# Optimization experiments

Measured on AMD Instinct MI355X. Metric: run time of the kernel, lower is better.

Reference implementation:

```python
import jax, jax.numpy as jnp
import numpy as np

N = 200000          # total nodes
G = 512             # num graphs (segments)
D = 256             # in_dim == h_dim == sum_dim
OUT = 128           # head out_dim
L = 4               # depth
EPS = 1e-5


def setup_inputs() -> dict:
    key = jax.random.key(0)
    ks = jax.random.split(key, 12)
    x = jax.random.normal(ks[0], (N, D), dtype=jnp.float32)
    batch = jnp.sort(jax.random.randint(ks[1], (N,), 0, G)).astype(jnp.int32)
    s = 0.06  # ~xavier scale for 256-wide layers
    return {
        "x": x,
        "batch": batch,
        "phi_w1": s * jax.random.normal(ks[2], (L, D, D), dtype=jnp.float32),
        "phi_b1": jnp.zeros((L, D), jnp.float32),
        "phi_ln_g": jnp.ones((L, D), jnp.float32),
        "phi_ln_b": jnp.zeros((L, D), jnp.float32),
        "phi_w2": s * jax.random.normal(ks[3], (L, D, D), dtype=jnp.float32),
        "phi_b2": jnp.zeros((L, D), jnp.float32),
        "psi_w1": s * jax.random.normal(ks[4], (L, 2 * D, D), dtype=jnp.float32),
        "psi_b1": jnp.zeros((L, D), jnp.float32),
        "psi_ln_g": jnp.ones((L, D), jnp.float32),
        "psi_ln_b": jnp.zeros((L, D), jnp.float32),
        "psi_w2": s * jax.random.normal(ks[5], (L, D, D), dtype=jnp.float32),
        "psi_b2": jnp.zeros((L, D), jnp.float32),
        "out_ln_g": jnp.ones((L, D), jnp.float32),
        "out_ln_b": jnp.zeros((L, D), jnp.float32),
        "head_w": s * jax.random.normal(ks[6], (D, OUT), dtype=jnp.float32),
        "head_b": jnp.zeros((OUT,), jnp.float32),
    }


def _ln(h, g, b):
    mu = jnp.mean(h, axis=-1, keepdims=True)
    var = jnp.mean(jnp.square(h - mu), axis=-1, keepdims=True)
    return (h - mu) * jax.lax.rsqrt(var + EPS) * g + b


def _mlp(h, w1, b1, g, beta, w2, b2):
    # Linear -> ReLU -> LayerNorm -> Linear (MLP with num_layers=2, use_ln=True)
    h = jax.nn.relu(h @ w1 + b1)
    h = _ln(h, g, beta)
    return h @ w2 + b2


def reference(x, batch, phi_w1, phi_b1, phi_ln_g, phi_ln_b, phi_w2, phi_b2,
              psi_w1, psi_b1, psi_ln_g, psi_ln_b, psi_w2, psi_b2,
              out_ln_g, out_ln_b, head_w, head_b):
    for i in range(L):
        phi_x = _mlp(x, phi_w1[i], phi_b1[i], phi_ln_g[i], phi_ln_b[i], phi_w2[i], phi_b2[i])
        # global_add_pool: scatter-add per graph, then gather back to nodes
        gsum = jax.ops.segment_sum(phi_x, batch, num_segments=G)   # [G, D]
        expanded = gsum[batch]                                      # [N, D]
        combined = jnp.concatenate([x, expanded], axis=-1)          # [N, 2D]
        out = _mlp(combined, psi_w1[i], psi_b1[i], psi_ln_g[i], psi_ln_b[i], psi_w2[i], psi_b2[i])
        out = x + out                                               # residual (in_dim == out_dim)
        x = _ln(out, out_ln_g[i], out_ln_b[i])                      # out_ln
    return x @ head_w + head_b
```

## Files before the change

### kernel.cpp

```cpp
#include <hip/hip_runtime.h>
#include <stdint.h>

#define DEV __device__ __forceinline__

constexpr int NN = 200000;
constexpr int GSEG = 512;

typedef __attribute__((ext_vector_type(8)))  short   s8v;
typedef __attribute__((ext_vector_type(4)))  float   f4v;
typedef __attribute__((ext_vector_type(16))) float   f16v;
typedef __attribute__((ext_vector_type(4)))  unsigned short u4v;
typedef __attribute__((ext_vector_type(4)))  _Float16 h4v;

DEV void mfma32(const s8v& a, const s8v& b, f16v& c){
  asm volatile("v_mfma_f32_32x32x16_bf16 %0, %1, %2, %0" : "+v"(c) : "v"(a), "v"(b));
}

DEV unsigned short f2bs(float f){
  union { float f; uint32_t u; } v; v.f = f;
  uint32_t u = v.u;
  u = u + 0x7fffu + ((u >> 16) & 1u);
  return (unsigned short)(u >> 16);
}
DEV float b2f(unsigned short s){
  union { uint32_t u; float f; } v; v.u = ((uint32_t)s) << 16;
  return v.f;
}
DEV unsigned short f2h(float f){
  union{ _Float16 h; unsigned short u; } v; v.h = (_Float16)f; return v.u;
}
DEV s8v cvt8(f4v a, f4v b){
  s8v r;
  r[0]=(short)f2bs(a[0]); r[1]=(short)f2bs(a[1]); r[2]=(short)f2bs(a[2]); r[3]=(short)f2bs(a[3]);
  r[4]=(short)f2bs(b[0]); r[5]=(short)f2bs(b[1]); r[6]=(short)f2bs(b[2]); r[7]=(short)f2bs(b[3]);
  return r;
}

DEV void gload_lds16(const void* g, void* l){
  __builtin_amdgcn_global_load_lds(
      (const __attribute__((address_space(1))) void*)g,
      (__attribute__((address_space(3))) void*)l, 16, 0, 0);
}

template<int BSRC>
DEV s8v load_bfrag(const unsigned short* Xb, const float* Xf, const float* gsum,
                   int row, int g, int kk, int k16){
  if constexpr(BSRC==0){
    return *(const s8v*)(Xb + (size_t)row*256 + kk);
  } else if constexpr(BSRC==1){
    const float* p = Xf + (size_t)row*256 + kk;
    return cvt8(*(const f4v*)p, *(const f4v*)(p+4));
  } else {
    if(k16 < 16){
      if constexpr(BSRC==2){
        return *(const s8v*)(Xb + (size_t)row*256 + kk);
      } else {
        const float* p = Xf + (size_t)row*256 + kk;
        return cvt8(*(const f4v*)p, *(const f4v*)(p+4));
      }
    } else {
      const float* p = gsum + (size_t)g*256 + (kk - 256);
      return cvt8(*(const f4v*)p, *(const f4v*)(p+4));
    }
  }
}

template<int DOUT,int KDIM,int BSRC,int MODE,int RES,int WRH>
__global__ __launch_bounds__(256,2) void gemm_ln(
    const unsigned short* Xb, const float* Xf, const float* gsumIn, const int* batch,
    const unsigned short* PW, const float* bias, const float* lng, const float* lnb,
    const float* xresf, const unsigned short* xresh, const unsigned short* xresb,
    unsigned short* outb, unsigned short* outh, float* outf)
{
  constexpr int NM  = DOUT/32;
  constexpr int NI  = DOUT/64;
  constexpr int CHB = NM*4096;
  constexpr int ITER= CHB/4096;
  __shared__ __align__(16) char smem[CHB + 2048];
  __shared__ __align__(16) char sT[32768];

  const int tid  = threadIdx.x;
  const int lane = tid & 63;
  const int wid  = tid >> 6;
  const int wr = wid >> 1, wc = wid & 1;
  const int l32 = lane & 31, h = lane >> 5;
  const int rb   = (int)blockIdx.x * 128;
  const int row0 = rb + wr*64 + l32;
  const int row1 = row0 + 32;
  const int r0c = row0 < NN ? row0 : NN-1;
  const int r1c = row1 < NN ? row1 : NN-1;

  f16v acc[2][NI];
  #pragma unroll
  for(int ni=0; ni<NI; ++ni){
    #pragma unroll
    for(int rq=0; rq<4; ++rq){
      f4v bv = *(const f4v*)(bias + wc*(DOUT/2) + ni*32 + 8*rq + 4*h);
      #pragma unroll
      for(int j=0;j<4;++j){ acc[0][ni][rq*4+j]=bv[j]; acc[1][ni][rq*4+j]=bv[j]; }
    }
  }

  int g0=0, g1=0;
  if constexpr(BSRC>=2){ g0 = batch[r0c]; g1 = batch[r1c]; }

  for(int kc=0; kc<KDIM/64; ++kc){
    const unsigned short* src = PW + (size_t)kc*(CHB/2);
    #pragma unroll
    for(int it=0; it<ITER; ++it){
      int idx = it*256 + tid;
      gload_lds16(src + (size_t)idx*8, smem + (it*256 + wid*64)*16);
    }
    __syncthreads();
    #pragma unroll
    for(int k2=0;k2<4;++k2){
      const int k16 = kc*4 + k2;
      const int kk  = k16*16 + h*8;
      s8v b0 = load_bfrag<BSRC>(Xb, Xf, gsumIn, r0c, g0, kk, k16);
      s8v b1 = load_bfrag<BSRC>(Xb, Xf, gsumIn, r1c, g1, kk, k16);
      #pragma unroll
      for(int ni=0; ni<NI; ++ni){
        s8v a = *(const s8v*)(smem + ((k2*NM + wc*NI + ni)*64 + lane)*16);
        mfma32(a, b0, acc[0][ni]);
        mfma32(a, b1, acc[1][ni]);
      }
    }
    __syncthreads();
  }

  if constexpr(MODE==0 || MODE==1){
    #pragma unroll
    for(int nj=0;nj<2;++nj){
      if constexpr(MODE==1){
        const int rr = nj ? r1c : r0c;
        #pragma unroll
        for(int ni=0;ni<NI;++ni){
          #pragma unroll
          for(int rq=0;rq<4;++rq){
            const int c4 = wc*(DOUT/2) + ni*32 + 8*rq + 4*h;
            f4v rv;
            if constexpr(RES==1){
              rv = *(const f4v*)(xresf + (size_t)rr*256 + c4);
            } else if constexpr(RES==2){
              h4v hv = *(const h4v*)(xresh + (size_t)rr*256 + c4);
              #pragma unroll
              for(int j=0;j<4;++j) rv[j] = (float)hv[j];
            } else {
              u4v u = *(const u4v*)(xresb + (size_t)rr*256 + c4);
              #pragma unroll
              for(int j=0;j<4;++j) rv[j] = b2f(u[j]);
            }
            #pragma unroll
            for(int j=0;j<4;++j) acc[nj][ni][rq*4+j] += rv[j];
          }
        }
      } else {
        #pragma unroll
        for(int ni=0;ni<NI;++ni)
          #pragma unroll
          for(int r=0;r<16;++r) acc[nj][ni][r] = fmaxf(acc[nj][ni][r], 0.f);
      }
    }
    float s[2]={0.f,0.f}, q[2]={0.f,0.f};
    #pragma unroll
    for(int nj=0;nj<2;++nj)
      #pragma unroll
      for(int ni=0;ni<NI;++ni)
        #pragma unroll
        for(int r=0;r<16;++r){ float v = acc[nj][ni][r]; s[nj]+=v; q[nj]=fmaf(v,v,q[nj]); }
    #pragma unroll
    for(int nj=0;nj<2;++nj){ s[nj] += __shfl_xor(s[nj],32); q[nj] += __shfl_xor(q[nj],32); }
    float2* st = (float2*)(smem + CHB);
    if(lane < 32){
      st[(((wr*2+0)*32)+lane)*2 + wc] = make_float2(s[0], q[0]);
      st[(((wr*2+1)*32)+lane)*2 + wc] = make_float2(s[1], q[1]);
    }
    __syncthreads();
    float mu[2], rs[2];
    #pragma unroll
    for(int nj=0;nj<2;++nj){
      f4v v = *(const f4v*)(st + (((wr*2+nj)*32)+l32)*2);
      float S = v[0]+v[2], Q = v[1]+v[3];
      mu[nj] = S*(1.f/256.f);
      float var = Q*(1.f/256.f) - mu[nj]*mu[nj];
      rs[nj] = rsqrtf(var + 1e-5f);
    }
    for(int chunk=0; chunk<2; ++chunk){
      if(chunk) __syncthreads();
      if(wr == chunk){
        #pragma unroll
        for(int nj=0;nj<2;++nj){
          #pragma unroll
          for(int ni=0;ni<NI;++ni){
            #pragma unroll
            for(int rq=0;rq<4;++rq){
              const int c4 = wc*(DOUT/2) + ni*32 + 8*rq + 4*h;
              f4v gv = *(const f4v*)(lng + c4);
              f4v bv = *(const f4v*)(lnb + c4);
              u4v o;
              #pragma unroll
              for(int j=0;j<4;++j)
                o[j] = f2bs(fmaf((acc[nj][ni][rq*4+j]-mu[nj])*rs[nj], gv[j], bv[j]));
              *(u4v*)(sT + (nj*32+l32)*512 + ((c4*2) ^ (l32<<4))) = o;
            }
          }
        }
      }
      __syncthreads();
      #pragma unroll
      for(int i=0;i<8;++i){
        const int r = i*8 + (tid>>5);
        const int c = tid & 31;
        const int grow = rb + chunk*64 + r;
        if(grow < NN)
          *(s8v*)(outb + (size_t)grow*256 + c*8) =
              *(const s8v*)(sT + r*512 + ((c*16) ^ ((r&31)<<4)));
      }
    }
    if constexpr(WRH){
      for(int chunk=0; chunk<2; ++chunk){
        __syncthreads();
        if(wr == chunk){
          #pragma unroll
          for(int nj=0;nj<2;++nj){
            #pragma unroll
            for(int ni=0;ni<NI;++ni){
              #pragma unroll
              for(int rq=0;rq<4;++rq){
                const int c4 = wc*(DOUT/2) + ni*32 + 8*rq + 4*h;
                f4v gv = *(const f4v*)(lng + c4);
                f4v bv = *(const f4v*)(lnb + c4);
                u4v o;
                #pragma unroll
                for(int j=0;j<4;++j)
                  o[j] = f2h(fmaf((acc[nj][ni][rq*4+j]-mu[nj])*rs[nj], gv[j], bv[j]));
                *(u4v*)(sT + (nj*32+l32)*512 + ((c4*2) ^ (l32<<4))) = o;
              }
            }
          }
        }
        __syncthreads();
        #pragma unroll
        for(int i=0;i<8;++i){
          const int r = i*8 + (tid>>5);
          const int c = tid & 31;
          const int grow = rb + chunk*64 + r;
          if(grow < NN)
            *(s8v*)(outh + (size_t)grow*256 + c*8) =
                *(const s8v*)(sT + r*512 + ((c*16) ^ ((r&31)<<4)));
        }
      }
    }
  } else {
    for(int chunk=0; chunk<2; ++chunk){
      if(chunk) __syncthreads();
      if(wr == chunk){
        #pragma unroll
        for(int nj=0;nj<2;++nj){
          #pragma unroll
          for(int ni=0;ni<NI;++ni){
            #pragma unroll
            for(int rq=0;rq<4;++rq){
              const int c4 = wc*(DOUT/2) + ni*32 + 8*rq + 4*h;
              f4v o;
              #pragma unroll
              for(int j=0;j<4;++j) o[j] = acc[nj][ni][rq*4+j];
              *(f4v*)(sT + (nj*32+l32)*512 + ((c4*4) ^ (l32<<4))) = o;
            }
          }
        }
      }
      __syncthreads();
      #pragma unroll
      for(int i=0;i<8;++i){
        const int r = i*8 + (tid>>5);
        const int c = tid & 31;
        const int grow = rb + chunk*64 + r;
        if(grow < NN)
          *(f4v*)(outf + (size_t)grow*DOUT + c*4) =
              *(const f4v*)(sT + r*512 + ((c*16) ^ ((r&31)<<4)));
      }
    }
  }
}

__global__ __launch_bounds__(256,2) void gemm_segsum(
    const unsigned short* Xb, const unsigned short* PW, const float* bias,
    const int* batch, float* gsum)
{
  __shared__ __align__(16) char smem[32768];
  const int tid = threadIdx.x, lane = tid&63, wid = tid>>6;
  const int wr = wid>>1, wc = wid&1, l32 = lane&31, h = lane>>5;
  const int rb = (int)blockIdx.x*128;
  const int ra0 = rb + wr*64 + l32;
  const int ra1 = ra0 + 32;
  const int r0c = ra0 < NN ? ra0 : NN-1;
  const int r1c = ra1 < NN ? ra1 : NN-1;
  const int browi = rb + wr*64 + lane;
  const int b_l = (browi < NN) ? batch[browi] : 0x7fffffff;

  f16v acc[2][4];
  #pragma unroll
  for(int n=0;n<4;++n){
    float bv = bias[wc*128 + n*32 + l32];
    #pragma unroll
    for(int m=0;m<2;++m)
      #pragma unroll
      for(int r=0;r<16;++r) acc[m][n][r] = bv;
  }

  for(int kc=0; kc<4; ++kc){
    const unsigned short* src = PW + (size_t)kc*16384;
    #pragma unroll
    for(int it=0; it<8; ++it){
      int idx = it*256 + tid;
      gload_lds16(src + (size_t)idx*8, smem + (it*256 + wid*64)*16);
    }
    __syncthreads();
    #pragma unroll
    for(int k2=0;k2<4;++k2){
      const int kk = (kc*4+k2)*16 + h*8;
      s8v a0 = *(const s8v*)(Xb + (size_t)r0c*256 + kk);
      s8v a1 = *(const s8v*)(Xb + (size_t)r1c*256 + kk);
      #pragma unroll
      for(int n=0;n<4;++n){
        s8v bw = *(const s8v*)(smem + ((k2*8 + wc*4 + n)*64 + lane)*16);
        mfma32(a0, bw, acc[0][n]);
        mfma32(a1, bw, acc[1][n]);
      }
    }
    __syncthreads();
  }

  int lo = 0;
  while(lo < 64){
    int g = __shfl(b_l, lo);
    unsigned long long mb = __ballot(b_l == g);
    int hi = lo + __popcll(mb);
    if(g < GSEG){
      #pragma unroll
      for(int n=0;n<4;++n){
        float sum = 0.f;
        #pragma unroll
        for(int m=0;m<2;++m){
          if(hi <= m*32 || lo >= m*32+32) continue;
          #pragma unroll
          for(int r=0;r<16;++r){
            int lr = m*32 + (r&3) + 8*(r>>2) + 4*h;
            sum += (lr >= lo && lr < hi) ? acc[m][n][r] : 0.f;
          }
        }
        sum += __shfl_xor(sum, 32);
        if(lane < 32) atomicAdd(&gsum[(size_t)g*256 + wc*128 + n*32 + lane], sum);
      }
    }
    lo = hi;
  }
}

__global__ void pack_weights(const float* phi_w1, const float* phi_w2,
                             const float* psi_w1, const float* psi_w2,
                             const float* head_w, unsigned short* pw)
{
  int o = (int)blockIdx.x*256 + (int)threadIdx.x;
  if(o >= 167936) return;
  const float* src; unsigned short* dst; int Dout, oo;
  if(o < 32768){        int l=o>>13;            oo=o&8191;  src=phi_w1+(size_t)l*65536;  dst=pw+(size_t)l*65536;           Dout=256; }
  else if(o < 65536){   int t=o-32768,l=t>>13;  oo=t&8191;  src=phi_w2+(size_t)l*65536;  dst=pw+262144+(size_t)l*65536;    Dout=256; }
  else if(o < 131072){  int t=o-65536,l=t>>14;  oo=t&16383; src=psi_w1+(size_t)l*131072; dst=pw+524288+(size_t)l*131072;   Dout=256; }
  else if(o < 163840){  int t=o-131072,l=t>>13; oo=t&8191;  src=psi_w2+(size_t)l*65536;  dst=pw+1048576+(size_t)l*65536;   Dout=256; }
  else{                 oo=o-163840;            src=head_w; dst=pw+1310720;                                                Dout=128; }
  const int NM = Dout/32;
  int lane = oo & 63;
  int m   = (oo>>6) % NM;
  int k16 = (oo>>6) / NM;
  int kb  = k16*16 + (lane>>5)*8;
  int col = m*32 + (lane&31);
  #pragma unroll
  for(int jj=0;jj<8;++jj) dst[(size_t)oo*8 + jj] = f2bs(src[(size_t)(kb+jj)*Dout + col]);
}

extern "C" void kernel_launch(void* const* d_in, const int* in_sizes, int n_in,
                              void* d_out, int out_size, void* d_ws, size_t ws_size,
                              hipStream_t stream)
{
  (void)in_sizes; (void)n_in; (void)out_size;
  const float* x0       = (const float*)d_in[0];
  const int*   batch    = (const int*)  d_in[1];
  const float* phi_w1   = (const float*)d_in[2];
  const float* phi_b1   = (const float*)d_in[3];
  const float* phi_ln_g = (const float*)d_in[4];
  const float* phi_ln_b = (const float*)d_in[5];
  const float* phi_w2   = (const float*)d_in[6];
  const float* phi_b2   = (const float*)d_in[7];
  const float* psi_w1   = (const float*)d_in[8];
  const float* psi_b1   = (const float*)d_in[9];
  const float* psi_ln_g = (const float*)d_in[10];
  const float* psi_ln_b = (const float*)d_in[11];
  const float* psi_w2   = (const float*)d_in[12];
  const float* psi_b2   = (const float*)d_in[13];
  const float* out_ln_g = (const float*)d_in[14];
  const float* out_ln_b = (const float*)d_in[15];
  const float* head_w   = (const float*)d_in[16];
  const float* head_b   = (const float*)d_in[17];

  char* ws = (char*)d_ws;
  unsigned short* pw = (unsigned short*)ws;
  float* gsum        = (float*)(ws + 4194304);
  unsigned short* hb = (unsigned short*)(ws + 8388608);
  const bool dual = (ws_size >= 315588608ull);
  unsigned short* xb = dual ? (unsigned short*)(ws + 110788608)
                            : (unsigned short*)d_out;
  unsigned short* xh = dual ? (unsigned short*)(ws + 213188608) : nullptr;

  const int grid = (NN + 127)/128;

  pack_weights<<<656,256,0,stream>>>(phi_w1, phi_w2, psi_w1, psi_w2, head_w, pw);

  for(int l=0;l<4;++l){
    const unsigned short* pw_phi1 = pw + (size_t)l*65536;
    const unsigned short* pw_phi2 = pw + 262144 + (size_t)l*65536;
    const unsigned short* pw_psi1 = pw + 524288 + (size_t)l*131072;
    const unsigned short* pw_psi2 = pw + 1048576 + (size_t)l*65536;
    const float* b1 = phi_b1 + l*256, *g1 = phi_ln_g + l*256, *n1 = phi_ln_b + l*256;
    const float* b2 = phi_b2 + l*256;
    const float* p1 = psi_b1 + l*256, *pg = psi_ln_g + l*256, *pn = psi_ln_b + l*256;
    const float* p2 = psi_b2 + l*256;
    const float* og = out_ln_g + l*256, *on = out_ln_b + l*256;

    if(l==0)
      gemm_ln<256,256,1,0,0,0><<<grid,256,0,stream>>>(nullptr, x0, nullptr, nullptr,
          pw_phi1, b1, g1, n1, nullptr, nullptr, nullptr, hb, nullptr, nullptr);
    else
      gemm_ln<256,256,0,0,0,0><<<grid,256,0,stream>>>(xb, nullptr, nullptr, nullptr,
          pw_phi1, b1, g1, n1, nullptr, nullptr, nullptr, hb, nullptr, nullptr);

    hipMemsetAsync(gsum, 0, 524288, stream);
    gemm_segsum<<<grid,256,0,stream>>>(hb, pw_phi2, b2, batch, gsum);

    if(l==0)
      gemm_ln<256,512,3,0,0,0><<<grid,256,0,stream>>>(nullptr, x0, gsum, batch,
          pw_psi1, p1, pg, pn, nullptr, nullptr, nullptr, hb, nullptr, nullptr);
    else
      gemm_ln<256,512,2,0,0,0><<<grid,256,0,stream>>>(xb, nullptr, gsum, batch,
          pw_psi1, p1, pg, pn, nullptr, nullptr, nullptr, hb, nullptr, nullptr);

    if(l==0){
      if(dual)
        gemm_ln<256,256,0,1,1,1><<<grid,256,0,stream>>>(hb, nullptr, nullptr, nullptr,
            pw_psi2, p2, og, on, x0, nullptr, nullptr, xb, xh, nullptr);
      else
        gemm_ln<256,256,0,1,1,0><<<grid,256,0,stream>>>(hb, nullptr, nullptr, nullptr,
            pw_psi2, p2, og, on, x0, nullptr, nullptr, xb, nullptr, nullptr);
    } else if(l<3){
      if(dual)
        gemm_ln<256,256,0,1,2,1><<<grid,256,0,stream>>>(hb, nullptr, nullptr, nullptr,
            pw_psi2, p2, og, on, nullptr, xh, nullptr, xb, xh, nullptr);
      else
        gemm_ln<256,256,0,1,3,0><<<grid,256,0,stream>>>(hb, nullptr, nullptr, nullptr,
            pw_psi2, p2, og, on, nullptr, nullptr, xb, xb, nullptr, nullptr);
    } else {
      if(dual)
        gemm_ln<256,256,0,1,2,0><<<grid,256,0,stream>>>(hb, nullptr, nullptr, nullptr,
            pw_psi2, p2, og, on, nullptr, xh, nullptr, xb, nullptr, nullptr);
      else
        gemm_ln<256,256,0,1,3,0><<<grid,256,0,stream>>>(hb, nullptr, nullptr, nullptr,
            pw_psi2, p2, og, on, nullptr, nullptr, xb, xb, nullptr, nullptr);
    }
  }

  gemm_ln<128,256,0,2,0,0><<<grid,256,0,stream>>>(xb, nullptr, nullptr, nullptr,
      pw + 1310720, head_b, nullptr, nullptr, nullptr, nullptr, nullptr,
      nullptr, nullptr, (float*)d_out);
}
```

Measured before the change: 1.698 ms.

## Store bf16/fp16 activations in MFMA-fragment tiled layout, drop LDS transpose epilogue

Intermediate bf16/fp16 activations move from row-major to a tiled layout (32-row blocks, 8-element column groups contiguous per row). B-fragment loads then become fully coalesced 512-byte runs, and the LN epilogue can write results straight from registers, pairing halves with a cross-lane shuffle. This removes the LDS staging buffer and its barriers in non-MODE2 kernels and cuts LDS usage, which may allow higher occupancy. The cost is that every producer and consumer must agree on the new layout, and the residual reads and other kernels have to be updated to match.

After: 1.516 ms. 10.7% less time.

```diff
diff --git a/kernel.cpp b/kernel.cpp
--- a/kernel.cpp
+++ b/kernel.cpp
@@ -42,26 +42,34 @@
       (__attribute__((address_space(3))) void*)l, 16, 0, 0);
 }
 
+DEV u4v shfl_xor32_u4(u4v v){
+  union { u4v q; long long l; } a, b;
+  a.q = v;
+  b.l = __shfl_xor(a.l, 32);
+  return b.q;
+}
+
+
 template<int BSRC>
 DEV s8v load_bfrag(const unsigned short* Xb, const float* Xf, const float* gsum,
-                   int row, int g, int kk, int k16){
+                   int row, int g, int k16, int h){
   if constexpr(BSRC==0){
-    return *(const s8v*)(Xb + (size_t)row*256 + kk);
+    return *(const s8v*)(Xb + (size_t)(row>>5)*8192 + (size_t)(k16*2+h)*256 + (row&31)*8);
   } else if constexpr(BSRC==1){
-    const float* p = Xf + (size_t)row*256 + kk;
+    const float* p = Xf + (size_t)row*256 + k16*16 + h*8;
+    return cvt8(*(const f4v*)p, *(const f4v*)(p+4));
+  } else if constexpr(BSRC==2){
+    if(k16 < 16)
+      return *(const s8v*)(Xb + (size_t)(row>>5)*8192 + (size_t)(k16*2+h)*256 + (row&31)*8);
+    const float* p = gsum + (size_t)g*256 + (k16-16)*16 + h*8;
     return cvt8(*(const f4v*)p, *(const f4v*)(p+4));
   } else {
     if(k16 < 16){
-      if constexpr(BSRC==2){
-        return *(const s8v*)(Xb + (size_t)row*256 + kk);
-      } else {
-        const float* p = Xf + (size_t)row*256 + kk;
-        return cvt8(*(const f4v*)p, *(const f4v*)(p+4));
-      }
-    } else {
-      const float* p = gsum + (size_t)g*256 + (kk - 256);
+      const float* p = Xf + (size_t)row*256 + k16*16 + h*8;
       return cvt8(*(const f4v*)p, *(const f4v*)(p+4));
     }
+    const float* p = gsum + (size_t)g*256 + (k16-16)*16 + h*8;
+    return cvt8(*(const f4v*)p, *(const f4v*)(p+4));
   }
 }
 
@@ -77,7 +85,7 @@
   constexpr int CHB = NM*4096;
   constexpr int ITER= CHB/4096;
   __shared__ __align__(16) char smem[CHB + 2048];
-  __shared__ __align__(16) char sT[32768];
+  __shared__ __align__(16) char sT[(MODE==2) ? 32768 : 16];
 
   const int tid  = threadIdx.x;
   const int lane = tid & 63;
@@ -115,9 +123,8 @@
     #pragma unroll
     for(int k2=0;k2<4;++k2){
       const int k16 = kc*4 + k2;
-      const int kk  = k16*16 + h*8;
-      s8v b0 = load_bfrag<BSRC>(Xb, Xf, gsumIn, r0c, g0, kk, k16);
-      s8v b1 = load_bfrag<BSRC>(Xb, Xf, gsumIn, r1c, g1, kk, k16);
+      s8v b0 = load_bfrag<BSRC>(Xb, Xf, gsumIn, r0c, g0, k16, h);
+      s8v b1 = load_bfrag<BSRC>(Xb, Xf, gsumIn, r1c, g1, k16, h);
       #pragma unroll
       for(int ni=0; ni<NI; ++ni){
         s8v a = *(const s8v*)(smem + ((k2*NM + wc*NI + ni)*64 + lane)*16);
@@ -142,11 +149,13 @@
             if constexpr(RES==1){
               rv = *(const f4v*)(xresf + (size_t)rr*256 + c4);
             } else if constexpr(RES==2){
-              h4v hv = *(const h4v*)(xresh + (size_t)rr*256 + c4);
+              const int o = wc*16 + ni*4 + rq;
+              h4v hv = *(const h4v*)(xresh + (size_t)(rr>>5)*8192 + (size_t)o*256 + (rr&31)*8 + 4*h);
               #pragma unroll
               for(int j=0;j<4;++j) rv[j] = (float)hv[j];
             } else {
-              u4v u = *(const u4v*)(xresb + (size_t)rr*256 + c4);
+              const int o = wc*16 + ni*4 + rq;
+              u4v u = *(const u4v*)(xresb + (size_t)(rr>>5)*8192 + (size_t)o*256 + (rr&31)*8 + 4*h);
               #pragma unroll
               for(int j=0;j<4;++j) rv[j] = b2f(u[j]);
             }
@@ -185,69 +194,61 @@
       float var = Q*(1.f/256.f) - mu[nj]*mu[nj];
       rs[nj] = rsqrtf(var + 1e-5f);
     }
-    for(int chunk=0; chunk<2; ++chunk){
-      if(chunk) __syncthreads();
-      if(wr == chunk){
-        #pragma unroll
-        for(int nj=0;nj<2;++nj){
-          #pragma unroll
-          for(int ni=0;ni<NI;++ni){
+    #pragma unroll
+    for(int nj=0;nj<2;++nj){
+      const int rowS = nj ? row1 : row0;
+      #pragma unroll
+      for(int t=0;t<8;++t){
+        const int niE = (16*t)>>5,     rqE = (2*t)&3;
+        const int niO = (16*t+8)>>5,   rqO = (2*t+1)&3;
+        f4v fe, fo;
+        {
+          const int c4 = wc*(DOUT/2) + niE*32 + 8*rqE + 4*h;
+          f4v gv = *(const f4v*)(lng + c4);
+          f4v bv = *(const f4v*)(lnb + c4);
+          #pragma unroll
+          for(int j=0;j<4;++j)
+            fe[j] = fmaf((acc[nj][niE][rqE*4+j]-mu[nj])*rs[nj], gv[j], bv[j]);
+        }
+        {
+          const int c4 = wc*(DOUT/2) + niO*32 + 8*rqO + 4*h;
+          f4v gv = *(const f4v*)(lng + c4);
+          f4v bv = *(const f4v*)(lnb + c4);
+          #pragma unroll
+          for(int j=0;j<4;++j)
+            fo[j] = fmaf((acc[nj][niO][rqO*4+j]-mu[nj])*rs[nj], gv[j], bv[j]);
+        }
+        const int o = wc*16 + 2*t + h;
+        unsigned short* dst = outb + (size_t)(rowS>>5)*8192 + (size_t)o*256 + (rowS&31)*8;
+        {
+          u4v qe, qo;
+          #pragma unroll
+          for(int j=0;j<4;++j){ qe[j] = f2bs(fe[j]); qo[j] = f2bs(fo[j]); }
+          u4v snd = h ? qe : qo;
+          u4v rcv = shfl_xor32_u4(snd);
+          u4v lo4 = h ? rcv : qe;
+          u4v hi4 = h ? qo  : rcv;
+          if(rowS < NN){
+            s8v ov;
             #pragma unroll
-            for(int rq=0;rq<4;++rq){
-              const int c4 = wc*(DOUT/2) + ni*32 + 8*rq + 4*h;
-              f4v gv = *(const f4v*)(lng + c4);
-              f4v bv = *(const f4v*)(lnb + c4);
-              u4v o;
-              #pragma unroll
-              for(int j=0;j<4;++j)
-                o[j] = f2bs(fmaf((acc[nj][ni][rq*4+j]-mu[nj])*rs[nj], gv[j], bv[j]));
-              *(u4v*)(sT + (nj*32+l32)*512 + ((c4*2) ^ (l32<<4))) = o;
-            }
+            for(int j=0;j<4;++j){ ov[j] = (short)lo4[j]; ov[4+j] = (short)hi4[j]; }
+            *(s8v*)dst = ov;
           }
         }
-      }
-      __syncthreads();
-      #pragma unroll
-      for(int i=0;i<8;++i){
-        const int r = i*8 + (tid>>5);
-        const int c = tid & 31;
-        const int grow = rb + chunk*64 + r;
-        if(grow < NN)
-          *(s8v*)(outb + (size_t)grow*256 + c*8) =
-              *(const s8v*)(sT + r*512 + ((c*16) ^ ((r&31)<<4)));
-      }
-    }
-    if constexpr(WRH){
-      for(int chunk=0; chunk<2; ++chunk){
-        __syncthreads();
-        if(wr == chunk){
-          #pragma unroll
-          for(int nj=0;nj<2;++nj){
+        if constexpr(WRH){
+          u4v qe, qo;
+          #pragma unroll
+          for(int j=0;j<4;++j){ qe[j] = f2h(fe[j]); qo[j] = f2h(fo[j]); }
+          u4v snd = h ? qe : qo;
+          u4v rcv = shfl_xor32_u4(snd);
+          u4v lo4 = h ? rcv : qe;
+          u4v hi4 = h ? qo  : rcv;
+          if(rowS < NN){
+            s8v ov;
             #pragma unroll
-            for(int ni=0;ni<NI;++ni){
-              #pragma unroll
-              for(int rq=0;rq<4;++rq){
-                const int c4 = wc*(DOUT/2) + ni*32 + 8*rq + 4*h;
-                f4v gv = *(const f4v*)(lng + c4);
-                f4v bv = *(const f4v*)(lnb + c4);
-                u4v o;
-                #pragma unroll
-                for(int j=0;j<4;++j)
-                  o[j] = f2h(fmaf((acc[nj][ni][rq*4+j]-mu[nj])*rs[nj], gv[j], bv[j]));
-                *(u4v*)(sT + (nj*32+l32)*512 + ((c4*2) ^ (l32<<4))) = o;
-              }
-            }
+            for(int j=0;j<4;++j){ ov[j] = (short)lo4[j]; ov[4+j] = (short)hi4[j]; }
+            *(s8v*)(outh + (size_t)(rowS>>5)*8192 + (size_t)o*256 + (rowS&31)*8) = ov;
           }
-        }
-        __syncthreads();
-        #pragma unroll
-        for(int i=0;i<8;++i){
-          const int r = i*8 + (tid>>5);
-          const int c = tid & 31;
-          const int grow = rb + chunk*64 + r;
-          if(grow < NN)
-            *(s8v*)(outh + (size_t)grow*256 + c*8) =
-                *(const s8v*)(sT + r*512 + ((c*16) ^ ((r&31)<<4)));
         }
       }
     }
@@ -319,9 +320,9 @@
     __syncthreads();
     #pragma unroll
     for(int k2=0;k2<4;++k2){
-      const int kk = (kc*4+k2)*16 + h*8;
-      s8v a0 = *(const s8v*)(Xb + (size_t)r0c*256 + kk);
-      s8v a1 = *(const s8v*)(Xb + (size_t)r1c*256 + kk);
+      const int k16 = kc*4+k2;
+      s8v a0 = *(const s8v*)(Xb + (size_t)(r0c>>5)*8192 + (size_t)(k16*2+h)*256 + (r0c&31)*8);
+      s8v a1 = *(const s8v*)(Xb + (size_t)(r1c>>5)*8192 + (size_t)(k16*2+h)*256 + (r1c&31)*8);
       #pragma unroll
       for(int n=0;n<4;++n){
         s8v bw = *(const s8v*)(smem + ((k2*8 + wc*4 + n)*64 + lane)*16);
```
